# Performance work log

Hardware: AMD Instinct MI355X
Metric: run time of the kernel (lower is better)

Reference implementation:

```python
import jax, jax.numpy as jnp
import numpy as np
import math

B, S, D = 2, 2048, 1024
H = 16
DK = D // H  # dim_k == dim_v == 64


def setup_inputs() -> dict:
    key = jax.random.key(0)
    ks = jax.random.split(key, 8)
    scale = 1.0 / math.sqrt(D)
    inp = {
        "query": jax.random.normal(ks[0], (B, S, D), dtype=jnp.float32),
        "key": jax.random.normal(ks[1], (B, S, D), dtype=jnp.float32),
        "value": jax.random.normal(ks[2], (B, S, D), dtype=jnp.float32),
        # stacked per-head projection weights (torch Linear y = x @ W.T; here stored as [H, D, DK])
        "Wq": jax.random.uniform(ks[3], (H, D, DK), dtype=jnp.float32, minval=-scale, maxval=scale),
        "Wk": jax.random.uniform(ks[4], (H, D, DK), dtype=jnp.float32, minval=-scale, maxval=scale),
        "Wv": jax.random.uniform(ks[5], (H, D, DK), dtype=jnp.float32, minval=-scale, maxval=scale),
        "Wo": jax.random.uniform(ks[6], (D, H * DK), dtype=jnp.float32, minval=-scale, maxval=scale),
        "bo": jax.random.uniform(ks[7], (D,), dtype=jnp.float32, minval=-scale, maxval=scale),
    }
    return inp


def reference(query, key, value, Wq, Wk, Wv, Wo, bo):
    # per-head projections, batched over heads via einsum
    q = jnp.einsum("bsd,hdk->bhsk", query, Wq)   # [B,H,S,DK]
    k = jnp.einsum("btd,hdk->bhtk", key, Wk)     # [B,H,S,DK]
    v = jnp.einsum("btd,hdv->bhtv", value, Wv)   # [B,H,S,DK]
    scores = jnp.einsum("bhsk,bhtk->bhst", q, k) / jnp.sqrt(jnp.float32(DK))
    # causal mask (is_causal=True): strictly upper triangle -> -inf
    causal = jnp.tril(jnp.ones((S, S), dtype=bool))  # True = keep
    scores = jnp.where(causal[None, None], scores, -jnp.inf)
    attn = jax.nn.softmax(scores, axis=-1)
    # NaN correction (no-op under pure causal masking, kept for faithfulness)
    attn = jnp.where(jnp.isnan(attn), 0.0, attn)
    out = jnp.einsum("bhst,bhtv->bhsv", attn, v)  # [B,H,S,DK]
    out = jnp.transpose(out, (0, 2, 1, 3)).reshape(B, S, H * DK)  # concat heads
    return out @ Wo.T + bo
```

## Files before the change

### kernel.cpp

```cpp
#include <hip/hip_runtime.h>


#define B_ 2
#define S_ 2048
#define D_ 1024
#define H_ 16
#define DK_ 64
#define NEG_BIG (-1e30f)

typedef unsigned short u16;
typedef __attribute__((ext_vector_type(8))) short bf16x8;
typedef __attribute__((ext_vector_type(4))) float f32x4;

__device__ __forceinline__ float b2f(u16 v) {
    union { unsigned u; float f; } x; x.u = ((unsigned)v) << 16; return x.f;
}
__device__ __forceinline__ u16 f2b(float f) {
    union { float f; unsigned u; } x; x.f = f;
    unsigned r = x.u + 0x7fff + ((x.u >> 16) & 1);
    return (u16)(r >> 16);
}
__device__ __forceinline__ u16 f2b_fast(float f) {
    union { float f; unsigned u; } x; x.f = f;
    return (u16)((x.u + 0x8000u) >> 16);
}

__device__ __forceinline__ bool is_f32(const void* p) {
    const unsigned* u = (const unsigned*)p;
    int cnt = 0;
#pragma unroll
    for (int i = 0; i < 64; i++) {
        unsigned e = (u[i * 8] >> 7) & 0xFFu;
        cnt += (e >= 110u && e <= 134u) ? 1 : 0;
    }
    return cnt < 32;
}

template<bool F32>
__device__ __forceinline__ bf16x8 load8(const void* p, size_t idx) {
    if constexpr (F32) {
        const float* f = (const float*)p + idx;
        float4 a = *(const float4*)f;
        float4 b = *(const float4*)(f + 4);
        bf16x8 r;
        ((u16*)&r)[0] = f2b(a.x); ((u16*)&r)[1] = f2b(a.y);
        ((u16*)&r)[2] = f2b(a.z); ((u16*)&r)[3] = f2b(a.w);
        ((u16*)&r)[4] = f2b(b.x); ((u16*)&r)[5] = f2b(b.y);
        ((u16*)&r)[6] = f2b(b.z); ((u16*)&r)[7] = f2b(b.w);
        return r;
    } else {
        return *(const bf16x8*)((const u16*)p + idx);
    }
}

__global__ __launch_bounds__(256) void wtrans(const void* Wq, const void* Wk, const void* Wv,
                                              u16* WqT, u16* WkT, u16* WvT) {
    __shared__ __align__(16) u16 Ts[64][72];
    const int t = threadIdx.x;
    const int k0 = blockIdx.x * 64;
    const int h = blockIdx.y;
    const int wsel = blockIdx.z;
    const void* W = (wsel == 0) ? Wq : (wsel == 1) ? Wk : Wv;
    u16* WT = (wsel == 0) ? WqT : (wsel == 1) ? WkT : WvT;
    const bool wf = is_f32(W);

    const int drow = t >> 2, c0 = (t & 3) * 16;
    size_t sidx = ((size_t)h * D_ + k0 + drow) * DK_ + c0;
    bf16x8 v0, v1;
    if (wf) { v0 = load8<true >(W, sidx); v1 = load8<true >(W, sidx + 8); }
    else    { v0 = load8<false>(W, sidx); v1 = load8<false>(W, sidx + 8); }
    *(bf16x8*)&Ts[drow][c0]     = v0;
    *(bf16x8*)&Ts[drow][c0 + 8] = v1;
    __syncthreads();

    const int nrow = t >> 2, kc0 = (t & 3) * 16;
    u16 tmp[16];
#pragma unroll
    for (int j = 0; j < 16; j++) tmp[j] = Ts[kc0 + j][nrow];
    u16* dst = &WT[((size_t)h * DK_ + nrow) * D_ + k0 + kc0];
    *(bf16x8*)&dst[0] = *(const bf16x8*)&tmp[0];
    *(bf16x8*)&dst[8] = *(const bf16x8*)&tmp[8];
}

template<bool AF32>
__device__ void qproj_body(const void* A, const u16* WT, u16* Qt, int bb,
                           u16 (*As)[72], u16 (*Wt)[72]) {
    const int tid = threadIdx.x, mt = blockIdx.x, h = blockIdx.y;
    const int w = tid >> 6, lane = tid & 63, quad = lane >> 4, ln = lane & 15;
    const int s0 = mt * 64;
    const int row = tid >> 3, col = (tid & 7) * 8;
    const int row1 = row + 32;
    const int brow = tid >> 2, bc0 = (tid & 3) * 16;
    const size_t wbase = ((size_t)h * DK_ + brow) * D_ + bc0;

    bf16x8 areg0, areg1, breg0, breg1;
    areg0 = load8<AF32>(A, ((size_t)bb * S_ + s0 + row ) * D_ + col);
    areg1 = load8<AF32>(A, ((size_t)bb * S_ + s0 + row1) * D_ + col);
    breg0 = *(const bf16x8*)&WT[wbase];
    breg1 = *(const bf16x8*)&WT[wbase + 8];

    f32x4 acc[4];
#pragma unroll
    for (int t = 0; t < 4; t++)
#pragma unroll
        for (int r = 0; r < 4; r++) acc[t][r] = 0.f;

    for (int k0 = 0; k0 < D_; k0 += 64) {
        *(bf16x8*)&As[row ][col] = areg0;
        *(bf16x8*)&As[row1][col] = areg1;
        *(bf16x8*)&Wt[brow][bc0    ] = breg0;
        *(bf16x8*)&Wt[brow][bc0 + 8] = breg1;
        __syncthreads();
        if (k0 + 64 < D_) {
            areg0 = load8<AF32>(A, ((size_t)bb * S_ + s0 + row ) * D_ + k0 + 64 + col);
            areg1 = load8<AF32>(A, ((size_t)bb * S_ + s0 + row1) * D_ + k0 + 64 + col);
            breg0 = *(const bf16x8*)&WT[wbase + k0 + 64];
            breg1 = *(const bf16x8*)&WT[wbase + k0 + 64 + 8];
        }
#pragma unroll
        for (int kk = 0; kk < 2; kk++) {
            bf16x8 a = *(const bf16x8*)&As[w * 16 + ln][kk * 32 + quad * 8];
#pragma unroll
            for (int t = 0; t < 4; t++) {
                bf16x8 bm = *(const bf16x8*)&Wt[t * 16 + ln][kk * 32 + quad * 8];
                acc[t] = __builtin_amdgcn_mfma_f32_16x16x32_bf16(a, bm, acc[t], 0, 0, 0);
            }
        }
        __syncthreads();
    }

#pragma unroll
    for (int t = 0; t < 4; t++)
#pragma unroll
        for (int r = 0; r < 4; r++)
            Qt[((size_t)bb * S_ + s0 + w * 16 + quad * 4 + r) * D_ + h * DK_ + t * 16 + ln] =
                f2b(acc[t][r] * 0.125f);
}

__global__ __launch_bounds__(256) void qproj(const void* query, const u16* WqT, u16* Qt) {
    __shared__ __align__(16) u16 As[64][72];
    __shared__ __align__(16) u16 Wt[64][72];
    const int bb = blockIdx.z;
    if (is_f32(query)) qproj_body<true >(query, WqT, Qt, bb, As, Wt);
    else               qproj_body<false>(query, WqT, Qt, bb, As, Wt);
}

template<bool AF32>
__device__ void projkv_body(const void* A, const u16* WT, u16* Ko, u16* VTo,
                            int bb, int which, u16 (*As)[72], u16 (*Wt)[72]) {
    const int tid = threadIdx.x, mt = blockIdx.x, h = blockIdx.y;
    const int w = tid >> 6, lane = tid & 63, quad = lane >> 4, ln = lane & 15;
    const int s0 = mt * 64;
    const int row = tid >> 3, col = (tid & 7) * 8;
    const int row1 = row + 32;
    const int brow = tid >> 2, bc0 = (tid & 3) * 16;
    const size_t wbase = ((size_t)h * DK_ + brow) * D_ + bc0;

    bf16x8 areg0, areg1, breg0, breg1;
    areg0 = load8<AF32>(A, ((size_t)bb * S_ + s0 + row ) * D_ + col);
    areg1 = load8<AF32>(A, ((size_t)bb * S_ + s0 + row1) * D_ + col);
    breg0 = *(const bf16x8*)&WT[wbase];
    breg1 = *(const bf16x8*)&WT[wbase + 8];

    f32x4 acc[4];
#pragma unroll
    for (int t = 0; t < 4; t++)
#pragma unroll
        for (int r = 0; r < 4; r++) acc[t][r] = 0.f;

    for (int k0 = 0; k0 < D_; k0 += 64) {
        *(bf16x8*)&As[row ][col] = areg0;
        *(bf16x8*)&As[row1][col] = areg1;
        *(bf16x8*)&Wt[brow][bc0    ] = breg0;
        *(bf16x8*)&Wt[brow][bc0 + 8] = breg1;
        __syncthreads();
        if (k0 + 64 < D_) {
            areg0 = load8<AF32>(A, ((size_t)bb * S_ + s0 + row ) * D_ + k0 + 64 + col);
            areg1 = load8<AF32>(A, ((size_t)bb * S_ + s0 + row1) * D_ + k0 + 64 + col);
            breg0 = *(const bf16x8*)&WT[wbase + k0 + 64];
            breg1 = *(const bf16x8*)&WT[wbase + k0 + 64 + 8];
        }
#pragma unroll
        for (int kk = 0; kk < 2; kk++) {
            bf16x8 a = *(const bf16x8*)&As[w * 16 + ln][kk * 32 + quad * 8];
#pragma unroll
            for (int t = 0; t < 4; t++) {
                bf16x8 bm = *(const bf16x8*)&Wt[t * 16 + ln][kk * 32 + quad * 8];
                acc[t] = __builtin_amdgcn_mfma_f32_16x16x32_bf16(a, bm, acc[t], 0, 0, 0);
            }
        }
        __syncthreads();
    }

    if (which == 0) {
#pragma unroll
        for (int t = 0; t < 4; t++)
#pragma unroll
            for (int r = 0; r < 4; r++)
                Ko[((size_t)h * S_ + s0 + w * 16 + quad * 4 + r) * DK_ + t * 16 + ln] =
                    f2b(acc[t][r]);
    } else {
#pragma unroll
        for (int t = 0; t < 4; t++)
#pragma unroll
            for (int r = 0; r < 4; r++)
                Wt[t * 16 + ln][w * 16 + quad * 4 + r] = f2b(acc[t][r]);
        __syncthreads();
        *(bf16x8*)&VTo[((size_t)h * DK_ + row ) * S_ + s0 + col] = *(const bf16x8*)&Wt[row ][col];
        *(bf16x8*)&VTo[((size_t)h * DK_ + row1) * S_ + s0 + col] = *(const bf16x8*)&Wt[row1][col];
    }
}

__global__ __launch_bounds__(256) void projkv(const void* key, const void* value,
                                              const u16* WkT, const u16* WvT,
                                              u16* KVbase, int bb) {
    __shared__ __align__(16) u16 As[64][72];
    __shared__ __align__(16) u16 Wt[64][72];
    const int which = blockIdx.z;
    const void* A = which ? value : key;
    const u16* WT = which ? WvT : WkT;
    u16* Ko  = KVbase;
    u16* VTo = KVbase + (size_t)H_ * S_ * DK_;
    if (is_f32(A)) projkv_body<true >(A, WT, Ko, VTo, bb, which, As, Wt);
    else           projkv_body<false>(A, WT, Ko, VTo, bb, which, As, Wt);
}

__global__ __launch_bounds__(256) void flashq(u16* __restrict__ Xq,
                                              const u16* __restrict__ KV,
                                              int bb0, size_t zstride) {
    __shared__ __align__(16) u16 BufA[64][72];
    __shared__ __align__(16) u16 BufB[64][72];
    __shared__ __align__(16) u16 Ps[4][16][72];
    const int tid = threadIdx.x;
    const int qt = (int)(gridDim.x - 1 - blockIdx.x);
    const int h = blockIdx.y;
    const int bb = bb0 + blockIdx.z;
    const u16* Kb  = KV + (size_t)blockIdx.z * zstride;
    const u16* VTb = Kb + (size_t)H_ * S_ * DK_;
    const int w = tid >> 6, lane = tid & 63, quad = lane >> 4, ln = lane & 15;
    const int s0 = qt * 64;
    const int row = tid >> 3, col = (tid & 7) * 8;
    const int row1 = row + 32;

    bf16x8 kreg0, kreg1, vreg0, vreg1;
    kreg0 = *(const bf16x8*)&Kb [((size_t)h * S_  + row ) * DK_ + col];
    kreg1 = *(const bf16x8*)&Kb [((size_t)h * S_  + row1) * DK_ + col];
    vreg0 = *(const bf16x8*)&VTb[((size_t)h * DK_ + row ) * S_  + col];
    vreg1 = *(const bf16x8*)&VTb[((size_t)h * DK_ + row1) * S_  + col];

    *(bf16x8*)&BufA[row ][col] = *(const bf16x8*)&Xq[((size_t)bb * S_ + s0 + row ) * D_ + h * DK_ + col];
    *(bf16x8*)&BufA[row1][col] = *(const bf16x8*)&Xq[((size_t)bb * S_ + s0 + row1) * D_ + h * DK_ + col];
    __syncthreads();
    bf16x8 qa0 = *(const bf16x8*)&BufA[w * 16 + ln][quad * 8];
    bf16x8 qa1 = *(const bf16x8*)&BufA[w * 16 + ln][32 + quad * 8];
    __syncthreads();

    f32x4 O[4];
    float psum[4];
#pragma unroll
    for (int t = 0; t < 4; t++)
#pragma unroll
        for (int r = 0; r < 4; r++) O[t][r] = 0.f;
#pragma unroll
    for (int r = 0; r < 4; r++) psum[r] = 0.f;

    for (int j = 0; j <= qt; j++) {
        *(bf16x8*)&BufA[row ][col] = kreg0;
        *(bf16x8*)&BufA[row1][col] = kreg1;
        *(bf16x8*)&BufB[row ][col] = vreg0;
        *(bf16x8*)&BufB[row1][col] = vreg1;
        __syncthreads();

        if (j < qt) {
            kreg0 = *(const bf16x8*)&Kb [((size_t)h * S_  + (j + 1) * 64 + row ) * DK_ + col];
            kreg1 = *(const bf16x8*)&Kb [((size_t)h * S_  + (j + 1) * 64 + row1) * DK_ + col];
            vreg0 = *(const bf16x8*)&VTb[((size_t)h * DK_ + row ) * S_ + (j + 1) * 64 + col];
            vreg1 = *(const bf16x8*)&VTb[((size_t)h * DK_ + row1) * S_ + (j + 1) * 64 + col];
        }

        f32x4 sf[4];
#pragma unroll
        for (int t = 0; t < 4; t++)
#pragma unroll
            for (int r = 0; r < 4; r++) sf[t][r] = 0.f;
#pragma unroll
        for (int kk = 0; kk < 2; kk++) {
            bf16x8 a = kk ? qa1 : qa0;
#pragma unroll
            for (int t = 0; t < 4; t++) {
                bf16x8 bm = *(const bf16x8*)&BufA[t * 16 + ln][kk * 32 + quad * 8];
                sf[t] = __builtin_amdgcn_mfma_f32_16x16x32_bf16(a, bm, sf[t], 0, 0, 0);
            }
        }

        if (j == qt) {
#pragma unroll
            for (int t = 0; t < 4; t++) {
                int keyl = t * 16 + ln;
#pragma unroll
                for (int r = 0; r < 4; r++) {
                    int qr = w * 16 + quad * 4 + r;
                    if (keyl > qr) sf[t][r] = NEG_BIG;
                }
            }
        }

#pragma unroll
        for (int t = 0; t < 4; t++)
#pragma unroll
            for (int r = 0; r < 4; r++) {
                float p = __expf(sf[t][r]);
                psum[r] += p;
                Ps[w][quad * 4 + r][t * 16 + ln] = f2b_fast(p);
            }
        __syncthreads();

#pragma unroll
        for (int kk = 0; kk < 2; kk++) {
            bf16x8 a = *(const bf16x8*)&Ps[w][ln][kk * 32 + quad * 8];
#pragma unroll
            for (int t = 0; t < 4; t++) {
                bf16x8 bm = *(const bf16x8*)&BufB[t * 16 + ln][kk * 32 + quad * 8];
                O[t] = __builtin_amdgcn_mfma_f32_16x16x32_bf16(a, bm, O[t], 0, 0, 0);
            }
        }
        __syncthreads();
    }

#pragma unroll
    for (int r = 0; r < 4; r++) {
        float s = psum[r];
        s += __shfl_xor(s, 1, 64);
        s += __shfl_xor(s, 2, 64);
        s += __shfl_xor(s, 4, 64);
        s += __shfl_xor(s, 8, 64);
        float inv = 1.0f / s;
        int sr = s0 + w * 16 + quad * 4 + r;
#pragma unroll
        for (int t = 0; t < 4; t++) {
            Xq[((size_t)bb * S_ + sr) * D_ + h * DK_ + t * 16 + ln] = f2b(O[t][r] * inv);
        }
    }
}

__global__ __launch_bounds__(256) void copyx(const u16* __restrict__ src,
                                             u16* __restrict__ dst) {
    size_t i = ((size_t)blockIdx.x * 256 + threadIdx.x) * 8;
    *(bf16x8*)&dst[i] = *(const bf16x8*)&src[i];
}

template<bool WF32>
__device__ void outgemm_body(const u16* X, const void* Wo, const void* bo, bool bf32,
                             float* Y, u16 (*As)[72], u16 (*Bs)[72]) {
    const int tid = threadIdx.x, mt = blockIdx.x, nt = blockIdx.y;
    const int w = tid >> 6, lane = tid & 63, quad = lane >> 4, ln = lane & 15;
    const int m0 = mt * 64, n0 = nt * 64;
    const int row = tid >> 3, col = (tid & 7) * 8;
    const int row1 = row + 32;

    bf16x8 areg0, areg1, wreg0, wreg1;
    areg0 = *(const bf16x8*)&X[(size_t)(m0 + row ) * D_ + col];
    areg1 = *(const bf16x8*)&X[(size_t)(m0 + row1) * D_ + col];
    wreg0 = load8<WF32>(Wo, (size_t)(n0 + row ) * D_ + col);
    wreg1 = load8<WF32>(Wo, (size_t)(n0 + row1) * D_ + col);

    f32x4 acc[4];
#pragma unroll
    for (int t = 0; t < 4; t++)
#pragma unroll
        for (int r = 0; r < 4; r++) acc[t][r] = 0.f;

    for (int k0 = 0; k0 < D_; k0 += 64) {
        *(bf16x8*)&As[row ][col] = areg0;
        *(bf16x8*)&As[row1][col] = areg1;
        *(bf16x8*)&Bs[row ][col] = wreg0;
        *(bf16x8*)&Bs[row1][col] = wreg1;
        __syncthreads();
        if (k0 + 64 < D_) {
            areg0 = *(const bf16x8*)&X[(size_t)(m0 + row ) * D_ + k0 + 64 + col];
            areg1 = *(const bf16x8*)&X[(size_t)(m0 + row1) * D_ + k0 + 64 + col];
            wreg0 = load8<WF32>(Wo, (size_t)(n0 + row ) * D_ + k0 + 64 + col);
            wreg1 = load8<WF32>(Wo, (size_t)(n0 + row1) * D_ + k0 + 64 + col);
        }
#pragma unroll
        for (int kk = 0; kk < 2; kk++) {
            bf16x8 a = *(const bf16x8*)&As[w * 16 + ln][kk * 32 + quad * 8];
#pragma unroll
            for (int t = 0; t < 4; t++) {
                bf16x8 bm = *(const bf16x8*)&Bs[t * 16 + ln][kk * 32 + quad * 8];
                acc[t] = __builtin_amdgcn_mfma_f32_16x16x32_bf16(a, bm, acc[t], 0, 0, 0);
            }
        }
        __syncthreads();
    }

#pragma unroll
    for (int t = 0; t < 4; t++) {
        int n = n0 + t * 16 + ln;
        float bias = bf32 ? ((const float*)bo)[n] : b2f(((const u16*)bo)[n]);
#pragma unroll
        for (int r = 0; r < 4; r++) {
            int m = m0 + w * 16 + quad * 4 + r;
            Y[(size_t)m * D_ + n] = acc[t][r] + bias;
        }
    }
}

__global__ __launch_bounds__(256) void outgemm(const u16* __restrict__ X,
                                               const void* Wo, const void* bo,
                                               float* __restrict__ Y) {
    __shared__ __align__(16) u16 As[64][72];
    __shared__ __align__(16) u16 Bs[64][72];
    const bool wf = is_f32(Wo), bf = is_f32(bo);
    if (wf) outgemm_body<true >(X, Wo, bo, bf, Y, As, Bs);
    else    outgemm_body<false>(X, Wo, bo, bf, Y, As, Bs);
}

extern "C" void kernel_launch(void* const* d_in, const int* in_sizes, int n_in,
                              void* d_out, int out_size, void* d_ws, size_t ws_size,
                              hipStream_t stream) {
    const void* q  = d_in[0];
    const void* k  = d_in[1];
    const void* v  = d_in[2];
    const void* Wq = d_in[3];
    const void* Wk = d_in[4];
    const void* Wv = d_in[5];
    const void* Wo = d_in[6];
    const void* bo = d_in[7];

    u16* ob   = (u16*)d_out;
    u16* Xq   = ob;
    u16* WkT  = ob + (size_t)4 * 1024 * 1024;
    u16* WvT  = WkT + (size_t)1024 * 1024;
    u16* WqT  = WvT + (size_t)1024 * 1024;
    u16* ws16 = (u16*)d_ws;
    const size_t kvblk = (size_t)2 * H_ * S_ * DK_;
    const bool bigws = ws_size >= (size_t)16 * 1024 * 1024;

    wtrans<<<dim3(D_ / 64, H_, 3), dim3(256), 0, stream>>>(Wq, Wk, Wv, WqT, WkT, WvT);
    qproj<<<dim3(S_ / 64, H_, B_), dim3(256), 0, stream>>>(q, WqT, Xq);
    if (bigws) {
        projkv<<<dim3(S_ / 64, H_, 2), dim3(256), 0, stream>>>(k, v, WkT, WvT, ws16, 0);
        projkv<<<dim3(S_ / 64, H_, 2), dim3(256), 0, stream>>>(k, v, WkT, WvT, ws16 + kvblk, 1);
        flashq<<<dim3(S_ / 64, H_, 2), dim3(256), 0, stream>>>(Xq, ws16, 0, kvblk);
    } else {
        projkv<<<dim3(S_ / 64, H_, 2), dim3(256), 0, stream>>>(k, v, WkT, WvT, ws16, 0);
        flashq<<<dim3(S_ / 64, H_, 1), dim3(256), 0, stream>>>(Xq, ws16, 0, 0);
        projkv<<<dim3(S_ / 64, H_, 2), dim3(256), 0, stream>>>(k, v, WkT, WvT, ws16, 1);
        flashq<<<dim3(S_ / 64, H_, 1), dim3(256), 0, stream>>>(Xq, ws16, 1, 0);
    }
    copyx<<<dim3((B_ * S_ * D_) / (256 * 8)), dim3(256), 0, stream>>>(Xq, ws16);
    outgemm<<<dim3((B_ * S_) / 64, D_ / 64), dim3(256), 0, stream>>>(ws16, Wo, bo, (float*)d_out);
}
```

Baseline: 291.4 us.

## Process two 64-row query tiles per flash-attention block to reuse K/V loads

Each flashq block now handles 128 query rows as two 64-row sub-tiles that share every K/V tile staged into shared memory, halving the grid along the sequence axis. The lower sub-tile skips the final key tile, and each sub-tile applies the causal mask on its own diagonal tile. Block order is reversed on alternate z-slices to spread long and short causal blocks across the grid. This cuts global K/V traffic and barrier count per query row, at the cost of more registers, fewer blocks (less parallelism), and larger per-block imbalance.

```diff
diff --git a/kernel.cpp b/kernel.cpp
--- a/kernel.cpp
+++ b/kernel.cpp
@@ -230,98 +230,155 @@
                                               int bb0, size_t zstride) {
     __shared__ __align__(16) u16 BufA[64][72];
     __shared__ __align__(16) u16 BufB[64][72];
-    __shared__ __align__(16) u16 Ps[4][16][72];
+    __shared__ __align__(16) u16 Ps[4][32][72];
     const int tid = threadIdx.x;
-    const int qt = (int)(gridDim.x - 1 - blockIdx.x);
+    const int bx = (int)blockIdx.x;
+    const int qt = (blockIdx.z & 1) ? bx : ((int)gridDim.x - 1 - bx);
     const int h = blockIdx.y;
     const int bb = bb0 + blockIdx.z;
     const u16* Kb  = KV + (size_t)blockIdx.z * zstride;
     const u16* VTb = Kb + (size_t)H_ * S_ * DK_;
     const int w = tid >> 6, lane = tid & 63, quad = lane >> 4, ln = lane & 15;
-    const int s0 = qt * 64;
+    const int s0 = qt * 128;
     const int row = tid >> 3, col = (tid & 7) * 8;
     const int row1 = row + 32;
-
-    bf16x8 kreg0, kreg1, vreg0, vreg1;
-    kreg0 = *(const bf16x8*)&Kb [((size_t)h * S_  + row ) * DK_ + col];
-    kreg1 = *(const bf16x8*)&Kb [((size_t)h * S_  + row1) * DK_ + col];
-    vreg0 = *(const bf16x8*)&VTb[((size_t)h * DK_ + row ) * S_  + col];
-    vreg1 = *(const bf16x8*)&VTb[((size_t)h * DK_ + row1) * S_  + col];
+    const int j0max = 2 * qt;
+    const int jmax  = 2 * qt + 1;
+
+    bf16x8 kreg0 = *(const bf16x8*)&Kb [((size_t)h * S_  + row ) * DK_ + col];
+    bf16x8 kreg1 = *(const bf16x8*)&Kb [((size_t)h * S_  + row1) * DK_ + col];
+    bf16x8 vreg0 = *(const bf16x8*)&VTb[((size_t)h * DK_ + row ) * S_  + col];
+    bf16x8 vreg1 = *(const bf16x8*)&VTb[((size_t)h * DK_ + row1) * S_  + col];
 
     *(bf16x8*)&BufA[row ][col] = *(const bf16x8*)&Xq[((size_t)bb * S_ + s0 + row ) * D_ + h * DK_ + col];
     *(bf16x8*)&BufA[row1][col] = *(const bf16x8*)&Xq[((size_t)bb * S_ + s0 + row1) * D_ + h * DK_ + col];
     __syncthreads();
-    bf16x8 qa0 = *(const bf16x8*)&BufA[w * 16 + ln][quad * 8];
-    bf16x8 qa1 = *(const bf16x8*)&BufA[w * 16 + ln][32 + quad * 8];
+    bf16x8 qa0_0 = *(const bf16x8*)&BufA[w * 16 + ln][quad * 8];
+    bf16x8 qa1_0 = *(const bf16x8*)&BufA[w * 16 + ln][32 + quad * 8];
     __syncthreads();
-
-    f32x4 O[4];
-    float psum[4];
+    *(bf16x8*)&BufA[row ][col] = *(const bf16x8*)&Xq[((size_t)bb * S_ + s0 + 64 + row ) * D_ + h * DK_ + col];
+    *(bf16x8*)&BufA[row1][col] = *(const bf16x8*)&Xq[((size_t)bb * S_ + s0 + 64 + row1) * D_ + h * DK_ + col];
+    __syncthreads();
+    bf16x8 qa0_1 = *(const bf16x8*)&BufA[w * 16 + ln][quad * 8];
+    bf16x8 qa1_1 = *(const bf16x8*)&BufA[w * 16 + ln][32 + quad * 8];
+    __syncthreads();
+
+    f32x4 O0[4], O1[4];
+    float psum0[4], psum1[4];
 #pragma unroll
     for (int t = 0; t < 4; t++)
 #pragma unroll
-        for (int r = 0; r < 4; r++) O[t][r] = 0.f;
-#pragma unroll
-    for (int r = 0; r < 4; r++) psum[r] = 0.f;
-
-    for (int j = 0; j <= qt; j++) {
+        for (int r = 0; r < 4; r++) { O0[t][r] = 0.f; O1[t][r] = 0.f; }
+#pragma unroll
+    for (int r = 0; r < 4; r++) { psum0[r] = 0.f; psum1[r] = 0.f; }
+
+    for (int j = 0; j <= jmax; j++) {
         *(bf16x8*)&BufA[row ][col] = kreg0;
         *(bf16x8*)&BufA[row1][col] = kreg1;
         *(bf16x8*)&BufB[row ][col] = vreg0;
         *(bf16x8*)&BufB[row1][col] = vreg1;
         __syncthreads();
 
-        if (j < qt) {
+        if (j < jmax) {
             kreg0 = *(const bf16x8*)&Kb [((size_t)h * S_  + (j + 1) * 64 + row ) * DK_ + col];
             kreg1 = *(const bf16x8*)&Kb [((size_t)h * S_  + (j + 1) * 64 + row1) * DK_ + col];
             vreg0 = *(const bf16x8*)&VTb[((size_t)h * DK_ + row ) * S_ + (j + 1) * 64 + col];
             vreg1 = *(const bf16x8*)&VTb[((size_t)h * DK_ + row1) * S_ + (j + 1) * 64 + col];
         }
 
-        f32x4 sf[4];
-#pragma unroll
-        for (int t = 0; t < 4; t++)
-#pragma unroll
-            for (int r = 0; r < 4; r++) sf[t][r] = 0.f;
+        const bool act0 = (j <= j0max);
+
+        if (act0) {
+            f32x4 sf[4];
+#pragma unroll
+            for (int t = 0; t < 4; t++)
+#pragma unroll
+                for (int r = 0; r < 4; r++) sf[t][r] = 0.f;
+#pragma unroll
+            for (int kk = 0; kk < 2; kk++) {
+                bf16x8 a = kk ? qa1_0 : qa0_0;
+#pragma unroll
+                for (int t = 0; t < 4; t++) {
+                    bf16x8 bm = *(const bf16x8*)&BufA[t * 16 + ln][kk * 32 + quad * 8];
+                    sf[t] = __builtin_amdgcn_mfma_f32_16x16x32_bf16(a, bm, sf[t], 0, 0, 0);
+                }
+            }
+            if (j == j0max) {
+#pragma unroll
+                for (int t = 0; t < 4; t++) {
+                    int keyl = t * 16 + ln;
+#pragma unroll
+                    for (int r = 0; r < 4; r++) {
+                        int qr = w * 16 + quad * 4 + r;
+                        if (keyl > qr) sf[t][r] = NEG_BIG;
+                    }
+                }
+            }
+#pragma unroll
+            for (int t = 0; t < 4; t++)
+#pragma unroll
+                for (int r = 0; r < 4; r++) {
+                    float p = __expf(sf[t][r]);
+                    psum0[r] += p;
+                    Ps[w][quad * 4 + r][t * 16 + ln] = f2b_fast(p);
+                }
+        }
+
+        {
+            f32x4 sf[4];
+#pragma unroll
+            for (int t = 0; t < 4; t++)
+#pragma unroll
+                for (int r = 0; r < 4; r++) sf[t][r] = 0.f;
+#pragma unroll
+            for (int kk = 0; kk < 2; kk++) {
+                bf16x8 a = kk ? qa1_1 : qa0_1;
+#pragma unroll
+                for (int t = 0; t < 4; t++) {
+                    bf16x8 bm = *(const bf16x8*)&BufA[t * 16 + ln][kk * 32 + quad * 8];
+                    sf[t] = __builtin_amdgcn_mfma_f32_16x16x32_bf16(a, bm, sf[t], 0, 0, 0);
+                }
+            }
+            if (j == jmax) {
+#pragma unroll
+                for (int t = 0; t < 4; t++) {
+                    int keyl = t * 16 + ln;
+#pragma unroll
+                    for (int r = 0; r < 4; r++) {
+                        int qr = w * 16 + quad * 4 + r;
+                        if (keyl > qr) sf[t][r] = NEG_BIG;
+                    }
+                }
+            }
+#pragma unroll
+            for (int t = 0; t < 4; t++)
+#pragma unroll
+                for (int r = 0; r < 4; r++) {
+                    float p = __expf(sf[t][r]);
+                    psum1[r] += p;
+                    Ps[w][16 + quad * 4 + r][t * 16 + ln] = f2b_fast(p);
+                }
+        }
+        __syncthreads();
+
+        if (act0) {
+#pragma unroll
+            for (int kk = 0; kk < 2; kk++) {
+                bf16x8 a = *(const bf16x8*)&Ps[w][ln][kk * 32 + quad * 8];
+#pragma unroll
+                for (int t = 0; t < 4; t++) {
+                    bf16x8 bm = *(const bf16x8*)&BufB[t * 16 + ln][kk * 32 + quad * 8];
+                    O0[t] = __builtin_amdgcn_mfma_f32_16x16x32_bf16(a, bm, O0[t], 0, 0, 0);
+                }
+            }
+        }
 #pragma unroll
         for (int kk = 0; kk < 2; kk++) {
-            bf16x8 a = kk ? qa1 : qa0;
-#pragma unroll
-            for (int t = 0; t < 4; t++) {
-                bf16x8 bm = *(const bf16x8*)&BufA[t * 16 + ln][kk * 32 + quad * 8];
-                sf[t] = __builtin_amdgcn_mfma_f32_16x16x32_bf16(a, bm, sf[t], 0, 0, 0);
-            }
-        }
-
-        if (j == qt) {
-#pragma unroll
-            for (int t = 0; t < 4; t++) {
-                int keyl = t * 16 + ln;
-#pragma unroll
-                for (int r = 0; r < 4; r++) {
-                    int qr = w * 16 + quad * 4 + r;
-                    if (keyl > qr) sf[t][r] = NEG_BIG;
-                }
-            }
-        }
-
-#pragma unroll
-        for (int t = 0; t < 4; t++)
-#pragma unroll
-            for (int r = 0; r < 4; r++) {
-                float p = __expf(sf[t][r]);
-                psum[r] += p;
-                Ps[w][quad * 4 + r][t * 16 + ln] = f2b_fast(p);
-            }
-        __syncthreads();
-
-#pragma unroll
-        for (int kk = 0; kk < 2; kk++) {
-            bf16x8 a = *(const bf16x8*)&Ps[w][ln][kk * 32 + quad * 8];
+            bf16x8 a = *(const bf16x8*)&Ps[w][16 + ln][kk * 32 + quad * 8];
 #pragma unroll
             for (int t = 0; t < 4; t++) {
                 bf16x8 bm = *(const bf16x8*)&BufB[t * 16 + ln][kk * 32 + quad * 8];
-                O[t] = __builtin_amdgcn_mfma_f32_16x16x32_bf16(a, bm, O[t], 0, 0, 0);
+                O1[t] = __builtin_amdgcn_mfma_f32_16x16x32_bf16(a, bm, O1[t], 0, 0, 0);
             }
         }
         __syncthreads();
@@ -329,7 +386,7 @@
 
 #pragma unroll
     for (int r = 0; r < 4; r++) {
-        float s = psum[r];
+        float s = psum0[r];
         s += __shfl_xor(s, 1, 64);
         s += __shfl_xor(s, 2, 64);
         s += __shfl_xor(s, 4, 64);
@@ -338,7 +395,21 @@
         int sr = s0 + w * 16 + quad * 4 + r;
 #pragma unroll
         for (int t = 0; t < 4; t++) {
-            Xq[((size_t)bb * S_ + sr) * D_ + h * DK_ + t * 16 + ln] = f2b(O[t][r] * inv);
+            Xq[((size_t)bb * S_ + sr) * D_ + h * DK_ + t * 16 + ln] = f2b(O0[t][r] * inv);
+        }
+    }
+#pragma unroll
+    for (int r = 0; r < 4; r++) {
+        float s = psum1[r];
+        s += __shfl_xor(s, 1, 64);
+        s += __shfl_xor(s, 2, 64);
+        s += __shfl_xor(s, 4, 64);
+        s += __shfl_xor(s, 8, 64);
+        float inv = 1.0f / s;
+        int sr = s0 + 64 + w * 16 + quad * 4 + r;
+#pragma unroll
+        for (int t = 0; t < 4; t++) {
+            Xq[((size_t)bb * S_ + sr) * D_ + h * DK_ + t * 16 + ln] = f2b(O1[t][r] * inv);
         }
     }
 }
@@ -442,12 +513,12 @@
     if (bigws) {
         projkv<<<dim3(S_ / 64, H_, 2), dim3(256), 0, stream>>>(k, v, WkT, WvT, ws16, 0);
         projkv<<<dim3(S_ / 64, H_, 2), dim3(256), 0, stream>>>(k, v, WkT, WvT, ws16 + kvblk, 1);
-        flashq<<<dim3(S_ / 64, H_, 2), dim3(256), 0, stream>>>(Xq, ws16, 0, kvblk);
+        flashq<<<dim3(S_ / 128, H_, 2), dim3(256), 0, stream>>>(Xq, ws16, 0, kvblk);
     } else {
         projkv<<<dim3(S_ / 64, H_, 2), dim3(256), 0, stream>>>(k, v, WkT, WvT, ws16, 0);
-        flashq<<<dim3(S_ / 64, H_, 1), dim3(256), 0, stream>>>(Xq, ws16, 0, 0);
+        flashq<<<dim3(S_ / 128, H_, 1), dim3(256), 0, stream>>>(Xq, ws16, 0, 0);
         projkv<<<dim3(S_ / 64, H_, 2), dim3(256), 0, stream>>>(k, v, WkT, WvT, ws16, 1);
-        flashq<<<dim3(S_ / 64, H_, 1), dim3(256), 0, stream>>>(Xq, ws16, 1, 0);
+        flashq<<<dim3(S_ / 128, H_, 1), dim3(256), 0, stream>>>(Xq, ws16, 1, 0);
     }
     copyx<<<dim3((B_ * S_ * D_) / (256 * 8)), dim3(256), 0, stream>>>(Xq, ws16);
     outgemm<<<dim3((B_ * S_) / 64, D_ / 64), dim3(256), 0, stream>>>(ws16, Wo, bo, (float*)d_out);
```

Result: no change. 288.1 us (-1.1%).
